# Kernel tuning notes

Measured on AMD Instinct MI355X. Metric: run time of the kernel, lower is better.

The kernel has to match this reference:

```python
import jax, jax.numpy as jnp
import numpy as np

DIM = 1024
N_HEADS = 16
HEAD_DIM = DIM // N_HEADS


def setup_inputs() -> dict:
    key = jax.random.key(0)
    k_x, k_qkv, k_out = jax.random.split(key, 3)
    B, L = 4, 2048
    x = jax.random.normal(k_x, (B, L, DIM), dtype=jnp.float32)
    # torch Linear weight has shape [out, in]; y = x @ W.T
    s = 1.0 / np.sqrt(DIM)
    W_qkv = jax.random.uniform(k_qkv, (3 * DIM, DIM), dtype=jnp.float32, minval=-s, maxval=s)
    W_out = jax.random.uniform(k_out, (DIM, DIM), dtype=jnp.float32, minval=-s, maxval=s)
    return {"x": x, "W_qkv": W_qkv, "W_out": W_out}


def reference(x, W_qkv, W_out):
    B, L, D = x.shape
    H, Hd = N_HEADS, HEAD_DIM
    scale = Hd ** (-0.5)
    qkv = x @ W_qkv.T                       # [B, L, 3D]
    q, k, v = jnp.split(qkv, 3, axis=-1)
    # 'b l (h d) -> b h l d'
    q = q.reshape(B, L, H, Hd).transpose(0, 2, 1, 3)
    k = k.reshape(B, L, H, Hd).transpose(0, 2, 1, 3)
    v = v.reshape(B, L, H, Hd).transpose(0, 2, 1, 3)
    attn = jnp.einsum('bhld,bhmd->bhlm', q, k) * scale  # [B, H, L, L]
    causal = jnp.tril(jnp.ones((L, L), dtype=bool))
    attn = jnp.where(causal, attn, -jnp.inf)
    attn = jax.nn.softmax(attn, axis=-1)
    out = jnp.einsum('bhlm,bhmd->bhld', attn, v)        # [B, H, L, Hd]
    out = out.transpose(0, 2, 1, 3).reshape(B, L, D)    # 'b h l d -> b l (h d)'
    return out @ W_out.T
```

## Files before the change

### kernel.cpp

```cpp
#include <hip/hip_runtime.h>
#include <stdint.h>

#define BATCH 4
#define SEQ   2048
#define DIM_  1024
#define NHEAD 16
#define HDIM  64

#define QSC 0.18033688011112042f

typedef __attribute__((ext_vector_type(8)))  short bf8;
typedef __attribute__((ext_vector_type(4)))  short s4v;
typedef __attribute__((ext_vector_type(4)))  float f4;
typedef __attribute__((ext_vector_type(16))) float f16v;
typedef __attribute__((ext_vector_type(2)))  unsigned int u2;
typedef __attribute__((ext_vector_type(4)))  unsigned int u4;

#define MFMA(a, b, c)   __builtin_amdgcn_mfma_f32_16x16x32_bf16(a, b, c, 0, 0, 0)
#define MFMA32(a, b, c) __builtin_amdgcn_mfma_f32_32x32x16_bf16(a, b, c, 0, 0, 0)

#define BAR_LGKM() asm volatile("s_waitcnt lgkmcnt(0)\n\ts_barrier" ::: "memory")
#define PBAR() asm volatile("s_barrier" ::: "memory")

static __device__ __forceinline__ short f2b(float f) {
    uint32_t u = __builtin_bit_cast(uint32_t, f);
    u = (u + 0x7FFFu + ((u >> 16) & 1u)) >> 16;
    return (short)u;
}

static __device__ __forceinline__ uint32_t cvtpk(float lo, float hi) {
    uint32_t r;
    asm("v_cvt_pk_bf16_f32 %0, %1, %2" : "=v"(r) : "v"(lo), "v"(hi));
    return r;
}

typedef const uint32_t __attribute__((address_space(1)))* gas_t;
typedef uint32_t __attribute__((address_space(3)))* las_t;
static __device__ __forceinline__ void gl_lds16(const short* g, short* l) {
    __builtin_amdgcn_global_load_lds((gas_t)g, (las_t)l, 16, 0, 0);
}

__global__ void cvt_all(const float* __restrict__ x, const float* __restrict__ wq,
                        const float* __restrict__ wo, short* __restrict__ xb,
                        short* __restrict__ wqb, short* __restrict__ wob) {
    const int NX = BATCH * SEQ * DIM_ / 4, NQ = 3 * DIM_ * DIM_ / 4;
    int i = blockIdx.x * blockDim.x + threadIdx.x;
    const float4* in; s4v* out; int j;
    if (i < NX)           { in = (const float4*)x;  out = (s4v*)xb;  j = i; }
    else if (i < NX + NQ) { in = (const float4*)wq; out = (s4v*)wqb; j = i - NX; }
    else                  { in = (const float4*)wo; out = (s4v*)wob; j = i - NX - NQ; }
    float4 v = in[j];
    s4v o;
    o.x = f2b(v.x); o.y = f2b(v.y); o.z = f2b(v.z); o.w = f2b(v.w);
    out[j] = o;
}

#define NT 16

#define PG_PROLOG()                                                           \
    __shared__ __align__(16) short lds[2 * 32768];                            \
    const int tid  = threadIdx.x;                                             \
    const int lane = tid & 63;                                                \
    const int wave = tid >> 6;                                                \
    const int quad = lane >> 4, l16 = lane & 15;                              \
    const int wr = wave >> 2, wc = wave & 3;                                  \
                     \
    const int gx  = gridDim.x;                                                \
    const int nwg = gx * gridDim.y;                                           \
    const int lid = blockIdx.y * gx + blockIdx.x;                             \
    const int swz = (lid & 7) * (nwg >> 3) + (lid >> 3);                      \
    const int m0 = (swz / gx) * 256;                                          \
    const int n0 = (swz % gx) * 256;                                          \
    const short* gA[4]; const short* gB[4]; int dA[4];                        \
    _Pragma("unroll") for (int j = 0; j < 4; ++j) {                           \
        const int idx = j * 512 + tid;                                        \
        const int row = idx >> 3, pos = idx & 7;                              \
        gA[j] = A + (size_t)(m0 + row) * 1024 + (pos ^ (row & 7)) * 8;        \
        gB[j] = W + (size_t)(n0 + row) * 1024 + (pos ^ (row & 7)) * 8;        \
        dA[j] = idx * 8;                                                      \
    }                                                                         \
    int aoff[8], boff[4];                                                     \
    _Pragma("unroll") for (int i = 0; i < 8; ++i)                             \
        aoff[i] = (wr * 128 + i * 16 + l16) * 64;                             \
    _Pragma("unroll") for (int i = 0; i < 4; ++i)                             \
        boff[i] = 16384 + (wc * 64 + i * 16 + l16) * 64;                      \
    const int kx  = l16 & 7;                                                  \
    const int kc0 = ((0 + quad) ^ kx) * 8;                                    \
    const int kc1 = ((4 + quad) ^ kx) * 8;                                    \
    short* cur = lds; short* nxt = lds + 32768;                               \
    f4 acc[8][4] = {};

#define PG_ISSUE_B01(bp) do { gl_lds16(gB[0], (bp) + 16384 + dA[0]);          \
                              gl_lds16(gB[1], (bp) + 16384 + dA[1]); } while (0)
#define PG_ISSUE_B23(bp) do { gl_lds16(gB[2], (bp) + 16384 + dA[2]);          \
                              gl_lds16(gB[3], (bp) + 16384 + dA[3]); } while (0)
#define PG_ISSUE_A(bp)   do { gl_lds16(gA[0], (bp) + dA[0]);                  \
                              gl_lds16(gA[2], (bp) + dA[2]);                  \
                              gl_lds16(gA[1], (bp) + dA[1]);                  \
                              gl_lds16(gA[3], (bp) + dA[3]); } while (0)
#define PG_BUMP() _Pragma("unroll") for (int j = 0; j < 4; ++j) { gA[j] += 64; gB[j] += 64; }

#define PG_MFMA16(ACCB, AV)                                                   \
    __builtin_amdgcn_s_setprio(1);                                            \
    _Pragma("unroll") for (int mt = 0; mt < 4; ++mt)                          \
        _Pragma("unroll") for (int nt = 0; nt < 4; ++nt)                      \
            acc[ACCB + mt][nt] = MFMA(AV[mt], b[nt], acc[ACCB + mt][nt]);     \
    __builtin_amdgcn_s_setprio(0);

#define PG_KLOOP()                                                            \
    PG_ISSUE_B01(cur); PG_ISSUE_B23(cur); PG_ISSUE_A(cur);                    \
    PG_BUMP();                                                                \
    asm volatile("s_waitcnt vmcnt(2)\n\ts_barrier" ::: "memory");             \
    for (int t = 0; t < NT; ++t) {                                            \
        const bool pre = (t < NT - 1);                                        \
        bf8 a[4], b[4];                                                       \
                                                \
        _Pragma("unroll") for (int i = 0; i < 4; ++i) {                       \
            a[i] = *(const bf8*)(cur + aoff[i] + kc0);                        \
            b[i] = *(const bf8*)(cur + boff[i] + kc0);                        \
        }                                                                     \
        if (pre) PG_ISSUE_B01(nxt);                                           \
        PBAR();                                                               \
        PG_MFMA16(0, a);                                                      \
                     \
        if (pre) asm volatile("s_waitcnt vmcnt(2)\n\ts_barrier" ::: "memory");\
        else     asm volatile("s_waitcnt vmcnt(0)\n\ts_barrier" ::: "memory");\
                                     \
        bf8 a2[4];                                                            \
        _Pragma("unroll") for (int i = 0; i < 4; ++i)                         \
            a2[i] = *(const bf8*)(cur + aoff[4 + i] + kc0);                   \
        if (pre) PG_ISSUE_B23(nxt);                                           \
        PBAR();                                                               \
        PG_MFMA16(4, a2);                                                     \
        PBAR();                                                               \
                                                \
        _Pragma("unroll") for (int i = 0; i < 4; ++i) {                       \
            a[i] = *(const bf8*)(cur + aoff[i] + kc1);                        \
            b[i] = *(const bf8*)(cur + boff[i] + kc1);                        \
        }                                                                     \
        if (pre) { PG_ISSUE_A(nxt); PG_BUMP(); }                              \
        PBAR();                                                               \
        PG_MFMA16(0, a);                                                      \
        PBAR();                                                               \
                                                \
        _Pragma("unroll") for (int i = 0; i < 4; ++i)                         \
            a2[i] = *(const bf8*)(cur + aoff[4 + i] + kc1);                   \
        PBAR();                                                               \
        PG_MFMA16(4, a2);                                                     \
               \
        if (pre) asm volatile("s_waitcnt vmcnt(2)\n\ts_barrier" ::: "memory");\
        short* tmp = cur; cur = nxt; nxt = tmp;                               \
    }

__global__ __launch_bounds__(512, 2) void gemm_qkv(const short* __restrict__ A,
                                                   const short* __restrict__ W,
                                                   short* __restrict__ Qd,
                                                   short* __restrict__ Kd,
                                                   short* __restrict__ Vd) {
    PG_PROLOG();
    PG_KLOOP();

    short* const bases[3] = {Qd, Kd, Vd};
    #pragma unroll
    for (int mf = 0; mf < 8; ++mf) {
        const int row = m0 + wr * 128 + mf * 16 + quad * 4;
        #pragma unroll
        for (int nf = 0; nf < 4; ++nf) {
            const int colb  = n0 + wc * 64 + nf * 16;
            const int which = colb >> 10;
            const int hh    = (colb >> 6) & 15;
            const int d0    = colb & 63;
            const float sc_ = (which == 0) ? QSC : 1.0f;
            short* bp = bases[which];
            #pragma unroll
            for (int r = 0; r < 4; ++r) {
                const int tk = row + r;
                const int bb = tk >> 11, ll = tk & 2047;
                bp[((size_t)(bb * NHEAD + hh) * SEQ + ll) * 64 + d0 + l16] =
                    f2b(acc[mf][nf][r] * sc_);
            }
        }
    }
}

__global__ __launch_bounds__(512, 2) void gemm_bt(const short* __restrict__ A,
                                                  const short* __restrict__ W,
                                                  float* __restrict__ Cp) {
    PG_PROLOG();
    PG_KLOOP();

    #pragma unroll
    for (int mf = 0; mf < 8; ++mf) {
        const int row = m0 + wr * 128 + mf * 16 + quad * 4;
        #pragma unroll
        for (int nf = 0; nf < 4; ++nf) {
            const int col = n0 + wc * 64 + nf * 16 + l16;
            #pragma unroll
            for (int r = 0; r < 4; ++r)
                Cp[(size_t)(row + r) * DIM_ + col] = acc[mf][nf][r];
        }
    }
}

__global__ __launch_bounds__(256) void flash_attn(const short* __restrict__ Qd,
                                                  const short* __restrict__ Kd,
                                                  const short* __restrict__ Vd,
                                                  short* __restrict__ out) {
    const int bh = blockIdx.x;
    const int b  = bh >> 4, h = bh & 15;
    const int qt = (gridDim.y - 1) - blockIdx.y;
    const int q0 = qt * 128;
    const int tid  = threadIdx.x;
    const int lane = tid & 63, wave = tid >> 6;
    const int l32  = lane & 31, khalf = lane >> 5;

    __shared__ __align__(16) short Ks[64 * 72];
    __shared__ __align__(16) short Vt[64 * 72];
    uint32_t* Vt32 = (uint32_t*)Vt;

    const short* Qp = Qd + (size_t)bh * (SEQ * 64);
    const short* Kp = Kd + (size_t)bh * (SEQ * 64);
    const short* Vp = Vd + (size_t)bh * (SEQ * 64);

    const int qrow = q0 + wave * 32 + l32;
    bf8 qf[4];
    #pragma unroll
    for (int dk = 0; dk < 4; ++dk)
        qf[dk] = *(const bf8*)(Qp + (size_t)qrow * 64 + dk * 16 + khalf * 8);

    const int skey = tid >> 2, sc = tid & 3;
    const int vkp = tid & 31, vds = (tid >> 5) * 8;

    bf8 ka0 = *(const bf8*)(Kp + (size_t)skey * 64 + sc * 8);
    bf8 ka1 = *(const bf8*)(Kp + (size_t)skey * 64 + (sc + 4) * 8);
    bf8 vr0 = *(const bf8*)(Vp + (size_t)(2 * vkp) * 64 + vds);
    bf8 vr1 = *(const bf8*)(Vp + (size_t)(2 * vkp + 1) * 64 + vds);

    f16v o0 = {}, o1 = {};
    float lsum = 0.f;
    const bf8 zz = {};

    const int nIter = 2 * qt + 2;
    for (int it = 0; it < nIter; ++it) {
        const int k0 = it * 64;

        BAR_LGKM();
        *(bf8*)(&Ks[skey * 72 + sc * 8])       = ka0;
        *(bf8*)(&Ks[skey * 72 + (sc + 4) * 8]) = ka1;
        #pragma unroll
        for (int i = 0; i < 8; ++i) {
            uint32_t p = (uint32_t)(uint16_t)vr0[i] | ((uint32_t)(uint16_t)vr1[i] << 16);
            Vt32[(vds + i) * 36 + vkp] = p;
        }
        BAR_LGKM();

        if (it + 1 < nIter) {
            const int kn = k0 + 64;
            ka0 = *(const bf8*)(Kp + (size_t)(kn + skey) * 64 + sc * 8);
            ka1 = *(const bf8*)(Kp + (size_t)(kn + skey) * 64 + (sc + 4) * 8);
            vr0 = *(const bf8*)(Vp + (size_t)(kn + 2 * vkp) * 64 + vds);
            vr1 = *(const bf8*)(Vp + (size_t)(kn + 2 * vkp + 1) * 64 + vds);
        }

        if (q0 + wave * 32 < k0) continue;

        bf8 pf[4];
        #pragma unroll
        for (int kt = 0; kt < 2; ++kt) {
            const int ktbase = k0 + kt * 32;
            const int rel = (q0 + wave * 32) - ktbase;
            if (rel < 0) {
                pf[kt * 2] = zz; pf[kt * 2 + 1] = zz;
                continue;
            }
            f16v st = {};
            __builtin_amdgcn_s_setprio(1);
            #pragma unroll
            for (int dk = 0; dk < 4; ++dk) {
                bf8 kf = *(const bf8*)(&Ks[(kt * 32 + l32) * 72 + dk * 16 + khalf * 8]);
                st = MFMA32(kf, qf[dk], st);
            }
            __builtin_amdgcn_s_setprio(0);
            float P[16];
            if (rel == 0) {
                #pragma unroll
                for (int r = 0; r < 16; ++r) {
                    const int kg = ktbase + (r & 3) + 8 * (r >> 2) + 4 * khalf;
                    float pv = __builtin_amdgcn_exp2f(st[r]);
                    P[r] = (kg > qrow) ? 0.0f : pv;
                }
            } else {
                #pragma unroll
                for (int r = 0; r < 16; ++r) P[r] = __builtin_amdgcn_exp2f(st[r]);
            }
            uint32_t w0 = cvtpk(P[0],  P[1]),  w1 = cvtpk(P[2],  P[3]);
            uint32_t w2 = cvtpk(P[4],  P[5]),  w3 = cvtpk(P[6],  P[7]);
            uint32_t w4 = cvtpk(P[8],  P[9]),  w5 = cvtpk(P[10], P[11]);
            uint32_t w6 = cvtpk(P[12], P[13]), w7 = cvtpk(P[14], P[15]);
            u2 s02 = __builtin_amdgcn_permlane32_swap(w0, w2, false, false);
            u2 s13 = __builtin_amdgcn_permlane32_swap(w1, w3, false, false);
            u2 s46 = __builtin_amdgcn_permlane32_swap(w4, w6, false, false);
            u2 s57 = __builtin_amdgcn_permlane32_swap(w5, w7, false, false);
            u4 q0w = {s02[0], s13[0], s02[1], s13[1]};
            u4 q1w = {s46[0], s57[0], s46[1], s57[1]};
            pf[kt * 2]     = __builtin_bit_cast(bf8, q0w);
            pf[kt * 2 + 1] = __builtin_bit_cast(bf8, q1w);
            float ls = ((P[0] + P[1]) + (P[2] + P[3])) +
                       ((P[4] + P[5]) + (P[6] + P[7])) +
                       ((P[8] + P[9]) + (P[10] + P[11])) +
                       ((P[12] + P[13]) + (P[14] + P[15]));
            lsum += ls;
        }

        __builtin_amdgcn_s_setprio(1);
        #pragma unroll
        for (int ks = 0; ks < 4; ++ks) {
            bf8 v0 = *(const bf8*)(&Vt[(l32) * 72 + ks * 16 + khalf * 8]);
            bf8 v1 = *(const bf8*)(&Vt[(32 + l32) * 72 + ks * 16 + khalf * 8]);
            o0 = MFMA32(pf[ks], v0, o0);
            o1 = MFMA32(pf[ks], v1, o1);
        }
        __builtin_amdgcn_s_setprio(0);
    }

    lsum += __shfl_xor(lsum, 32);
    short* outp = out + ((size_t)(b * SEQ + q0 + wave * 32) * DIM_) + h * 64;
    #pragma unroll
    for (int r = 0; r < 16; ++r) {
        const int rowl = (r & 3) + 8 * (r >> 2) + 4 * khalf;
        const float inv = 1.0f / __shfl(lsum, rowl);
        outp[(size_t)rowl * DIM_ + l32]      = f2b(o0[r] * inv);
        outp[(size_t)rowl * DIM_ + 32 + l32] = f2b(o1[r] * inv);
    }
}

extern "C" void kernel_launch(void* const* d_in, const int* in_sizes, int n_in,
                              void* d_out, int out_size, void* d_ws, size_t ws_size,
                              hipStream_t stream) {
    const float* x    = (const float*)d_in[0];
    const float* wqkv = (const float*)d_in[1];
    const float* wout = (const float*)d_in[2];

    char* ws = (char*)d_ws;
    short* xb    = (short*)(ws);
    short* wqkvb = (short*)(ws + (size_t)(16) * (1 << 20));
    short* woutb = (short*)(ws + (size_t)(22) * (1 << 20));
    short* Qd    = (short*)(ws + (size_t)(24) * (1 << 20));
    short* Kd    = (short*)(ws + (size_t)(40) * (1 << 20));
    short* Vd    = (short*)(ws + (size_t)(56) * (1 << 20));
    short* attnb = (short*)(ws + (size_t)(72) * (1 << 20));

    const int ntot = (BATCH * SEQ * DIM_ + 3 * DIM_ * DIM_ + DIM_ * DIM_) / 4;
    cvt_all<<<(ntot + 255) / 256, 256, 0, stream>>>(x, wqkv, wout, xb, wqkvb, woutb);

    gemm_qkv<<<dim3(3 * DIM_ / 256, BATCH * SEQ / 256), 512, 0, stream>>>(
        xb, wqkvb, Qd, Kd, Vd);

    flash_attn<<<dim3(BATCH * NHEAD, SEQ / 128), 256, 0, stream>>>(Qd, Kd, Vd, attnb);

    gemm_bt<<<dim3(DIM_ / 256, BATCH * SEQ / 256), 512, 0, stream>>>(
        attnb, woutb, (float*)d_out);
}
```

Baseline: 235.8 us.

## Split GEMM K-tile staging into half-tiles with deeper overlapped prefetch

```diff
diff --git a/kernel.cpp b/kernel.cpp
--- a/kernel.cpp
+++ b/kernel.cpp
@@ -55,50 +55,53 @@
     out[j] = o;
 }
 
-#define NT 16
+#define NT    16
+#define HREG  8192
+#define BUFS  32768
 
 #define PG_PROLOG()                                                           \
-    __shared__ __align__(16) short lds[2 * 32768];                            \
+    __shared__ __align__(16) short lds[2 * BUFS];                             \
     const int tid  = threadIdx.x;                                             \
     const int lane = tid & 63;                                                \
     const int wave = tid >> 6;                                                \
     const int quad = lane >> 4, l16 = lane & 15;                              \
     const int wr = wave >> 2, wc = wave & 3;                                  \
-                     \
     const int gx  = gridDim.x;                                                \
     const int nwg = gx * gridDim.y;                                           \
     const int lid = blockIdx.y * gx + blockIdx.x;                             \
     const int swz = (lid & 7) * (nwg >> 3) + (lid >> 3);                      \
     const int m0 = (swz / gx) * 256;                                          \
     const int n0 = (swz % gx) * 256;                                          \
-    const short* gA[4]; const short* gB[4]; int dA[4];                        \
-    _Pragma("unroll") for (int j = 0; j < 4; ++j) {                           \
+        \
+    const short* sgA[2]; const short* sgB[2]; int sld[2];                     \
+    _Pragma("unroll") for (int j = 0; j < 2; ++j) {                           \
         const int idx = j * 512 + tid;                                        \
-        const int row = idx >> 3, pos = idx & 7;                              \
-        gA[j] = A + (size_t)(m0 + row) * 1024 + (pos ^ (row & 7)) * 8;        \
-        gB[j] = W + (size_t)(n0 + row) * 1024 + (pos ^ (row & 7)) * 8;        \
-        dA[j] = idx * 8;                                                      \
+        const int row = idx >> 2, pos = idx & 3;                              \
+        const int c   = pos ^ ((row >> 1) & 3);                               \
+        sgA[j] = A + (size_t)(m0 + row) * 1024 + c * 8;                       \
+        sgB[j] = W + (size_t)(n0 + row) * 1024 + c * 8;                       \
+        sld[j] = idx * 8;                                                     \
     }                                                                         \
-    int aoff[8], boff[4];                                                     \
-    _Pragma("unroll") for (int i = 0; i < 8; ++i)                             \
-        aoff[i] = (wr * 128 + i * 16 + l16) * 64;                             \
-    _Pragma("unroll") for (int i = 0; i < 4; ++i)                             \
-        boff[i] = 16384 + (wc * 64 + i * 16 + l16) * 64;                      \
-    const int kx  = l16 & 7;                                                  \
-    const int kc0 = ((0 + quad) ^ kx) * 8;                                    \
-    const int kc1 = ((4 + quad) ^ kx) * 8;                                    \
-    short* cur = lds; short* nxt = lds + 32768;                               \
+                               \
+    int aoffs[8], boffs[4];                                                   \
+    _Pragma("unroll") for (int i = 0; i < 8; ++i) {                           \
+        const int rl = wr * 128 + i * 16 + l16;                               \
+        aoffs[i] = rl * 32 + (quad ^ ((rl >> 1) & 3)) * 8;                    \
+    }                                                                         \
+    _Pragma("unroll") for (int i = 0; i < 4; ++i) {                           \
+        const int cl = wc * 64 + i * 16 + l16;                                \
+        boffs[i] = 16384 + cl * 32 + (quad ^ ((cl >> 1) & 3)) * 8;            \
+    }                                                                         \
     f4 acc[8][4] = {};
 
-#define PG_ISSUE_B01(bp) do { gl_lds16(gB[0], (bp) + 16384 + dA[0]);          \
-                              gl_lds16(gB[1], (bp) + 16384 + dA[1]); } while (0)
-#define PG_ISSUE_B23(bp) do { gl_lds16(gB[2], (bp) + 16384 + dA[2]);          \
-                              gl_lds16(gB[3], (bp) + 16384 + dA[3]); } while (0)
-#define PG_ISSUE_A(bp)   do { gl_lds16(gA[0], (bp) + dA[0]);                  \
-                              gl_lds16(gA[2], (bp) + dA[2]);                  \
-                              gl_lds16(gA[1], (bp) + dA[1]);                  \
-                              gl_lds16(gA[3], (bp) + dA[3]); } while (0)
-#define PG_BUMP() _Pragma("unroll") for (int j = 0; j < 4; ++j) { gA[j] += 64; gB[j] += 64; }
+#define STG_A(bp, t, kh)                                                      \
+    do { const int ko = (t) * 64 + (kh) * 32;                                 \
+         gl_lds16(sgA[0] + ko, (bp) + (kh) * HREG + sld[0]);                  \
+         gl_lds16(sgA[1] + ko, (bp) + (kh) * HREG + sld[1]); } while (0)
+#define STG_B(bp, t, kh)                                                      \
+    do { const int ko = (t) * 64 + (kh) * 32;                                 \
+         gl_lds16(sgB[0] + ko, (bp) + 16384 + (kh) * HREG + sld[0]);          \
+         gl_lds16(sgB[1] + ko, (bp) + 16384 + (kh) * HREG + sld[1]); } while (0)
 
 #define PG_MFMA16(ACCB, AV)                                                   \
     __builtin_amdgcn_s_setprio(1);                                            \
@@ -108,48 +111,60 @@
     __builtin_amdgcn_s_setprio(0);
 
 #define PG_KLOOP()                                                            \
-    PG_ISSUE_B01(cur); PG_ISSUE_B23(cur); PG_ISSUE_A(cur);                    \
-    PG_BUMP();                                                                \
-    asm volatile("s_waitcnt vmcnt(2)\n\ts_barrier" ::: "memory");             \
-    for (int t = 0; t < NT; ++t) {                                            \
-        const bool pre = (t < NT - 1);                                        \
-        bf8 a[4], b[4];                                                       \
+    {                                                                         \
+        short* bf0 = lds; short* bf1 = lds + BUFS;                            \
+               \
+        STG_A(bf0, 0, 0); STG_B(bf0, 0, 0);                                   \
+        STG_A(bf0, 0, 1); STG_B(bf0, 0, 1);                                   \
+        STG_A(bf1, 1, 0); STG_B(bf1, 1, 0);                                   \
+        asm volatile("s_waitcnt vmcnt(8)\n\ts_barrier" ::: "memory");         \
+        short* cur = bf0; short* oth = bf1;                                   \
+        for (int t = 0; t < NT; ++t) {                                        \
+            bf8 a[4], a2[4], b[4];                                            \
                                                 \
-        _Pragma("unroll") for (int i = 0; i < 4; ++i) {                       \
-            a[i] = *(const bf8*)(cur + aoff[i] + kc0);                        \
-            b[i] = *(const bf8*)(cur + boff[i] + kc0);                        \
+            _Pragma("unroll") for (int i = 0; i < 4; ++i) {                   \
+                a[i] = *(const bf8*)(cur + aoffs[i]);                         \
+                b[i] = *(const bf8*)(cur + boffs[i]);                         \
+            }                                                                 \
+            if (t < NT - 1) STG_A(oth, t + 1, 1);                             \
+            PBAR();                                                           \
+            PG_MFMA16(0, a);                                                  \
+            PBAR();                                                           \
+                                     \
+            _Pragma("unroll") for (int i = 0; i < 4; ++i)                     \
+                a2[i] = *(const bf8*)(cur + aoffs[4 + i]);                    \
+            if (t < NT - 1) STG_B(oth, t + 1, 1);                             \
+            PBAR();                                                           \
+            PG_MFMA16(4, a2);                                                 \
+             \
+            if (t < NT - 1)                                                   \
+                asm volatile("s_waitcnt vmcnt(8)\n\ts_barrier" ::: "memory"); \
+            else                                                              \
+                asm volatile("s_waitcnt vmcnt(0)\n\ts_barrier" ::: "memory"); \
+                                                \
+            _Pragma("unroll") for (int i = 0; i < 4; ++i) {                   \
+                a[i] = *(const bf8*)(cur + HREG + aoffs[i]);                  \
+                b[i] = *(const bf8*)(cur + HREG + boffs[i]);                  \
+            }                                                                 \
+            if (t < NT - 2) STG_A(cur, t + 2, 0);                             \
+            PBAR();                                                           \
+            PG_MFMA16(0, a);                                                  \
+            PBAR();                                                           \
+                                                \
+            _Pragma("unroll") for (int i = 0; i < 4; ++i)                     \
+                a2[i] = *(const bf8*)(cur + HREG + aoffs[4 + i]);             \
+            if (t < NT - 2) STG_B(cur, t + 2, 0);                             \
+            PBAR();                                                           \
+            PG_MFMA16(4, a2);                                                 \
+                  \
+            if (t < NT - 2)                                                   \
+                asm volatile("s_waitcnt vmcnt(8)\n\ts_barrier" ::: "memory"); \
+            else if (t == NT - 2)                                             \
+                asm volatile("s_waitcnt vmcnt(4)\n\ts_barrier" ::: "memory"); \
+            else                                                              \
+                asm volatile("s_waitcnt vmcnt(0)\n\ts_barrier" ::: "memory"); \
+            short* tmp = cur; cur = oth; oth = tmp;                           \
         }                                                                     \
-        if (pre) PG_ISSUE_B01(nxt);                                           \
-        PBAR();                                                               \
-        PG_MFMA16(0, a);                                                      \
-                     \
-        if (pre) asm volatile("s_waitcnt vmcnt(2)\n\ts_barrier" ::: "memory");\
-        else     asm volatile("s_waitcnt vmcnt(0)\n\ts_barrier" ::: "memory");\
-                                     \
-        bf8 a2[4];                                                            \
-        _Pragma("unroll") for (int i = 0; i < 4; ++i)                         \
-            a2[i] = *(const bf8*)(cur + aoff[4 + i] + kc0);                   \
-        if (pre) PG_ISSUE_B23(nxt);                                           \
-        PBAR();                                                               \
-        PG_MFMA16(4, a2);                                                     \
-        PBAR();                                                               \
-                                                \
-        _Pragma("unroll") for (int i = 0; i < 4; ++i) {                       \
-            a[i] = *(const bf8*)(cur + aoff[i] + kc1);                        \
-            b[i] = *(const bf8*)(cur + boff[i] + kc1);                        \
-        }                                                                     \
-        if (pre) { PG_ISSUE_A(nxt); PG_BUMP(); }                              \
-        PBAR();                                                               \
-        PG_MFMA16(0, a);                                                      \
-        PBAR();                                                               \
-                                                \
-        _Pragma("unroll") for (int i = 0; i < 4; ++i)                         \
-            a2[i] = *(const bf8*)(cur + aoff[4 + i] + kc1);                   \
-        PBAR();                                                               \
-        PG_MFMA16(4, a2);                                                     \
-               \
-        if (pre) asm volatile("s_waitcnt vmcnt(2)\n\ts_barrier" ::: "memory");\
-        short* tmp = cur; cur = nxt; nxt = tmp;                               \
     }
 
 __global__ __launch_bounds__(512, 2) void gemm_qkv(const short* __restrict__ A,
```

Result: no change. 239.9 us (+1.7%).
